# Kernel tuning notes

Hardware: AMD Instinct MI355X
Metric: run time of the kernel (lower is better)

The kernel has to match this reference:

```python
import jax, jax.numpy as jnp
import numpy as np

H = 64; W = 64; P = 16; NPH = 4; NPW = 4; PH = 16; PW = 16; ZD = 32; HD = 1024; UD = 3; B = 256


def affine_grid(theta, Ho, Wo):
    # torch F.affine_grid, align_corners=False. theta [N,2,3] -> grid [N,Ho,Wo,2]
    xs = (2.0 * jnp.arange(Wo, dtype=theta.dtype) + 1.0) / Wo - 1.0
    ys = (2.0 * jnp.arange(Ho, dtype=theta.dtype) + 1.0) / Ho - 1.0
    X, Y = jnp.meshgrid(xs, ys)  # [Ho,Wo] each, x varies along last axis
    base = jnp.stack([X, Y, jnp.ones_like(X)], axis=-1)  # [Ho,Wo,3]
    return jnp.einsum('nij,hwj->nhwi', theta, base)


def grid_sample(img, grid):
    # torch F.grid_sample bilinear, padding_mode='zeros', align_corners=False
    # img [N,H,W], grid [N,Ho,Wo,2] in [-1,1]
    Hi, Wi = img.shape[1], img.shape[2]
    x = (grid[..., 0] + 1.0) * Wi / 2.0 - 0.5
    y = (grid[..., 1] + 1.0) * Hi / 2.0 - 0.5
    x0 = jnp.floor(x); y0 = jnp.floor(y)
    wx = x - x0; wy = y - y0

    def gather(ix, iy):
        valid = (ix >= 0) & (ix < Wi) & (iy >= 0) & (iy < Hi)
        ixc = jnp.clip(ix, 0, Wi - 1).astype(jnp.int32)
        iyc = jnp.clip(iy, 0, Hi - 1).astype(jnp.int32)
        v = jax.vmap(lambda im, yy, xx: im[yy, xx])(img, iyc, ixc)
        return jnp.where(valid, v, 0.0)

    return (gather(x0, y0) * (1 - wx) * (1 - wy)
            + gather(x0 + 1, y0) * wx * (1 - wy)
            + gather(x0, y0 + 1) * (1 - wx) * wy
            + gather(x0 + 1, y0 + 1) * wx * wy)


def rot_tr(u):
    # rotTrMatrix: u [N,3] (angle, tx, ty) -> [N,2,3]
    c = jnp.cos(u[:, 0]); s = jnp.sin(u[:, 0])
    R = jnp.stack([jnp.stack([c, -s], -1), jnp.stack([s, c], -1)], -2)  # [N,2,2]
    return jnp.concatenate([R, u[:, 1:3, None]], axis=2)


def anchor_theta():
    # anchor_move: identity rotation + per-part grid-cell-center translations
    tx = (np.arange(NPW) * (W / NPW) + W / NPW / 2) / W - 0.5
    ty = (np.arange(NPH) * (H / NPH) + H / NPH / 2) / H - 0.5
    th = np.tile(np.concatenate([np.eye(2), np.zeros((2, 1))], axis=1)[None], (P, 1, 1)).astype(np.float32)
    for k in range(P):
        th[k, 0, 2] = tx[k % NPW]
        th[k, 1, 2] = ty[k // NPW]
    return jnp.asarray(th)


def forward(inputs, W1, b1, W2, b2, Wum, bum, Wuv, buv, Wgm, bgm, Wgv, bgv, Wz, M, eps_u, eps_g):
    hid = jax.nn.relu(inputs.reshape(-1, H * W) @ W1 + b1)
    hid = jax.nn.relu(hid @ W2 + b2)
    # global transform distribution (note: F.threshold(x,-6,6) -> 6 where x<=-6)
    gmu = jnp.tanh(hid @ Wgm + bgm)
    gpre = hid @ Wgv + bgv
    gvar = jnp.exp(jnp.where(gpre > -6.0, gpre, 6.0))
    gu = gmu + gvar * eps_g  # sample_u uses mu + var*eps (var, not std) as in source
    # per-part transform distribution (F.threshold(x,-6,-6) -> clamp below at -6)
    umu = jnp.tanh(hid @ Wum + bum)
    upre = hid @ Wuv + buv
    uvar = jnp.exp(jnp.where(upre > -6.0, upre, -6.0))
    u = (umu + uvar * eps_u).reshape(-1, UD)  # [B*P,3]
    # decode parts (input is ones, as in source)
    parts = jax.nn.sigmoid(jnp.ones((B, ZD), inputs.dtype) @ Wz).reshape(B * P, PH, PW)
    padh = (H - PH) // 2; padw = (W - PW) // 2
    parts = jnp.pad(parts, ((0, 0), (padh, H - PH - padh), (padw, W - PW - padw)))
    # anchor placement of parts and kernel masks
    th_a = jnp.tile(anchor_theta(), (B, 1, 1))  # [B*P,2,3], part-minor ordering
    g_a = affine_grid(th_a, H, W)
    parts = grid_sample(parts, g_a)                     # [B*P,H,W]
    KM = grid_sample(M[:B * P].reshape(B * P, H, W), g_a)
    # per-part rotation+translation for parts; translation-only for kernel
    theta = rot_tr(u)                                   # [B*P,2,3]
    g = affine_grid(theta, H, W)
    eye = jnp.broadcast_to(jnp.eye(2, dtype=theta.dtype), (B * P, 2, 2))
    theta_K = jnp.concatenate([eye, theta[:, :, 2:3]], axis=2)
    g_K = affine_grid(theta_K, H, W)
    KM = grid_sample(KM, g_K).reshape(B, P, H, W)
    xp = grid_sample(parts, g).reshape(B, P, H, W)
    # masked weighted compositing
    num = jnp.sum(xp * KM, axis=1)
    den = jnp.sum(KM, axis=1)
    den = jnp.where(den == 0.0, 1.0, den)
    x = num / den
    # global transform
    theta_g = rot_tr(gu)
    g_g = affine_grid(theta_g, H, W)
    return grid_sample(x, g_g)[:, None]  # [B,1,H,W]


def setup_inputs() -> dict:
    key = jax.random.key(0)
    ks = jax.random.split(key, 18)

    def lin(k, fin, fout):
        return jax.random.normal(k, (fin, fout), jnp.float32) / np.sqrt(fin)

    return {
        'inputs': jax.random.uniform(ks[0], (B, H * W), jnp.float32),
        'W1': lin(ks[1], H * W, HD), 'b1': jnp.zeros((HD,), jnp.float32),
        'W2': lin(ks[2], HD, HD), 'b2': jnp.zeros((HD,), jnp.float32),
        'Wum': lin(ks[3], HD, P * UD), 'bum': jnp.zeros((P * UD,), jnp.float32),
        'Wuv': lin(ks[4], HD, P * UD), 'buv': jnp.zeros((P * UD,), jnp.float32),
        'Wgm': lin(ks[5], HD, UD), 'bgm': jnp.zeros((UD,), jnp.float32),
        'Wgv': lin(ks[6], HD, UD), 'bgv': jnp.zeros((UD,), jnp.float32),
        'Wz': lin(ks[7], ZD, P * PH * PW),
        'M': jax.random.uniform(ks[8], (B * P, 1, H, W), jnp.float32),
        'eps_u': jax.random.normal(ks[9], (B, P * UD), jnp.float32),
        'eps_g': jax.random.normal(ks[10], (B, UD), jnp.float32),
    }


def reference(inputs, W1, b1, W2, b2, Wum, bum, Wuv, buv, Wgm, bgm, Wgv, bgv, Wz, M, eps_u, eps_g):
    return forward(inputs, W1, b1, W2, b2, Wum, bum, Wuv, buv, Wgm, bgm, Wgv, bgv, Wz, M, eps_u, eps_g)
```

## Files before the change

kernel.cpp:

```cpp
#include <hip/hip_runtime.h>
#include <math.h>

#define SPLITK 8

typedef __bf16 bf16x8 __attribute__((ext_vector_type(8)));
typedef float  f32x4  __attribute__((ext_vector_type(4)));
typedef float  f32x16 __attribute__((ext_vector_type(16)));

__device__ inline unsigned short bf16rne(float x) {
    unsigned int u = __float_as_uint(x);
    unsigned int r = u + 0x7FFFu + ((u >> 16) & 1u);
    return (unsigned short)(r >> 16);
}
__device__ inline float bf16tof(unsigned short h) {
    return __uint_as_float(((unsigned int)h) << 16);
}

__global__ __launch_bounds__(256) void prep_all(
    const float* __restrict__ inputs,
    const float* __restrict__ W1, const float* __restrict__ W2,
    const float* __restrict__ Wum, const float* __restrict__ Wuv,
    const float* __restrict__ Wgm, const float* __restrict__ Wgv,
    const float* __restrict__ Wz,
    unsigned short* __restrict__ Ahi, unsigned short* __restrict__ Alo,
    unsigned short* __restrict__ W1Thi, unsigned short* __restrict__ W1Tlo,
    unsigned short* __restrict__ W2Thi, unsigned short* __restrict__ W2Tlo,
    float* __restrict__ WT, float* __restrict__ partsb)
{
    __shared__ float t[32][33];
    int bid = blockIdx.x;
    int tid = threadIdx.x;
    if (bid < 4096 || (bid >= 5120 && bid < 6144)) {
        const float* W = (bid < 4096) ? W1 : W2;
        unsigned short* Thi = (bid < 4096) ? W1Thi : W2Thi;
        unsigned short* Tlo = (bid < 4096) ? W1Tlo : W2Tlo;
        int K = (bid < 4096) ? 4096 : 1024;
        int b2 = (bid < 4096) ? bid : (bid - 5120);
        int n0 = (b2 & 31) * 32, k0 = (b2 >> 5) * 32;
        int c = tid & 31, r0 = tid >> 5;
#pragma unroll
        for (int i = 0; i < 4; i++)
            t[r0 + 8 * i][c] = W[(size_t)(k0 + r0 + 8 * i) * 1024 + n0 + c];
        __syncthreads();
        int kk = tid & 31, n1 = tid >> 5;
#pragma unroll
        for (int i = 0; i < 4; i++) {
            float x = t[kk][n1 + 8 * i];
            unsigned short h = bf16rne(x);
            unsigned short l = bf16rne(x - bf16tof(h));
            size_t o = (size_t)(n0 + n1 + 8 * i) * K + k0 + kk;
            Thi[o] = h;
            Tlo[o] = l;
        }
    } else if (bid < 5120) {
        int id = ((bid - 4096) * 256 + tid) * 4;
        float4 x = *(const float4*)(inputs + id);
        ushort4 h, l;
        h.x = bf16rne(x.x); l.x = bf16rne(x.x - bf16tof(h.x));
        h.y = bf16rne(x.y); l.y = bf16rne(x.y - bf16tof(h.y));
        h.z = bf16rne(x.z); l.z = bf16rne(x.z - bf16tof(h.z));
        h.w = bf16rne(x.w); l.w = bf16rne(x.w - bf16tof(h.w));
        *(ushort4*)(Ahi + id) = h;
        *(ushort4*)(Alo + id) = l;
    } else if (bid < 6552) {
        int id = (bid - 6144) * 256 + tid;
        int o = id >> 10;
        int k = id & 1023;
        float v;
        if (o < 48)       v = Wum[k * 48 + o];
        else if (o < 96)  v = Wuv[k * 48 + (o - 48)];
        else if (o < 99)  v = Wgm[k * 3 + (o - 96)];
        else              v = Wgv[k * 3 + (o - 99)];
        WT[id] = v;
    } else {
        int idx = (bid - 6552) * 256 + tid;
        float s = 0.f;
#pragma unroll
        for (int z = 0; z < 32; z++) s += Wz[z * 4096 + idx];
        partsb[idx] = 1.f / (1.f + expf(-s));
    }
}

__global__ __launch_bounds__(256) void gemm_bf16x3(
    const unsigned short* __restrict__ Ahi, const unsigned short* __restrict__ Alo,
    const unsigned short* __restrict__ Bhi, const unsigned short* __restrict__ Blo,
    float* __restrict__ psum, int K, int kchunk)
{
    __shared__ unsigned short Ah[4096], Al[4096], Bh[4096], Bl[4096];
    int tid = threadIdx.x;
    int n0 = blockIdx.x * 64, m0 = blockIdx.y * 64;
    int kb = blockIdx.z * kchunk;
    int wid = tid >> 6, lane = tid & 63;
    int wm = wid & 1, wn = wid >> 1;
    int lr = lane & 31, hi = lane >> 5;

    int r0 = tid >> 3, ch0 = tid & 7;
    int r1 = (tid + 256) >> 3, ch1 = (tid + 256) & 7;
    int l0 = r0 * 64 + 8 * (ch0 ^ (r0 & 7));
    int l1 = r1 * 64 + 8 * (ch1 ^ (r1 & 7));
    size_t ga0 = (size_t)(m0 + r0) * K + kb + ch0 * 8;
    size_t ga1 = (size_t)(m0 + r1) * K + kb + ch1 * 8;
    size_t gb0 = (size_t)(n0 + r0) * K + kb + ch0 * 8;
    size_t gb1 = (size_t)(n0 + r1) * K + kb + ch1 * 8;

    f32x16 acc_hh = {}, acc_hl = {}, acc_lh = {};

    int nkt = kchunk >> 6;
    uint4 vah0, vah1, val0, val1, vbh0, vbh1, vbl0, vbl1;
    vah0 = *(const uint4*)(Ahi + ga0);
    vah1 = *(const uint4*)(Ahi + ga1);
    val0 = *(const uint4*)(Alo + ga0);
    val1 = *(const uint4*)(Alo + ga1);
    vbh0 = *(const uint4*)(Bhi + gb0);
    vbh1 = *(const uint4*)(Bhi + gb1);
    vbl0 = *(const uint4*)(Blo + gb0);
    vbl1 = *(const uint4*)(Blo + gb1);

    int basea = (wm * 32 + lr) * 64;
    int baseb = (wn * 32 + lr) * 64;
    int sw = lr & 7;

    for (int kt = 0; kt < nkt; kt++) {
        __syncthreads();
        *(uint4*)(Ah + l0) = vah0;
        *(uint4*)(Ah + l1) = vah1;
        *(uint4*)(Al + l0) = val0;
        *(uint4*)(Al + l1) = val1;
        *(uint4*)(Bh + l0) = vbh0;
        *(uint4*)(Bh + l1) = vbh1;
        *(uint4*)(Bl + l0) = vbl0;
        *(uint4*)(Bl + l1) = vbl1;
        __syncthreads();
        if (kt + 1 < nkt) {
            size_t o = (size_t)(kt + 1) * 64;
            vah0 = *(const uint4*)(Ahi + ga0 + o);
            vah1 = *(const uint4*)(Ahi + ga1 + o);
            val0 = *(const uint4*)(Alo + ga0 + o);
            val1 = *(const uint4*)(Alo + ga1 + o);
            vbh0 = *(const uint4*)(Bhi + gb0 + o);
            vbh1 = *(const uint4*)(Bhi + gb1 + o);
            vbl0 = *(const uint4*)(Blo + gb0 + o);
            vbl1 = *(const uint4*)(Blo + gb1 + o);
        }
#pragma unroll
        for (int s = 0; s < 4; s++) {
            int cidx = 8 * (((s << 1) + hi) ^ sw);
            bf16x8 afh = *(const bf16x8*)(Ah + basea + cidx);
            bf16x8 afl = *(const bf16x8*)(Al + basea + cidx);
            bf16x8 bfh = *(const bf16x8*)(Bh + baseb + cidx);
            bf16x8 bfl = *(const bf16x8*)(Bl + baseb + cidx);
            acc_hh = __builtin_amdgcn_mfma_f32_32x32x16_bf16(afh, bfh, acc_hh, 0, 0, 0);
            acc_hl = __builtin_amdgcn_mfma_f32_32x32x16_bf16(afh, bfl, acc_hl, 0, 0, 0);
            acc_lh = __builtin_amdgcn_mfma_f32_32x32x16_bf16(afl, bfh, acc_lh, 0, 0, 0);
        }
    }

    float* op = psum + (size_t)blockIdx.z * (256 * 1024);
    int colg = n0 + wn * 32 + lr;
#pragma unroll
    for (int r = 0; r < 16; r++) {
        int rowl = (r & 3) + 8 * (r >> 2) + 4 * hi;
        float v = acc_hh[r] + acc_hl[r] + acc_lh[r];
        op[(size_t)(m0 + wm * 32 + rowl) * 1024 + colg] = v;
    }
}

__global__ __launch_bounds__(256) void reduce_bias_relu_split(
    const float* __restrict__ psum, const float* __restrict__ bias,
    unsigned short* __restrict__ hi, unsigned short* __restrict__ lo)
{
    int i = (blockIdx.x * 256 + threadIdx.x) * 4;
    float4 v = *(const float4*)(psum + i);
#pragma unroll
    for (int s = 1; s < SPLITK; s++) {
        float4 t = *(const float4*)(psum + (size_t)s * 262144 + i);
        v.x += t.x; v.y += t.y; v.z += t.z; v.w += t.w;
    }
    float4 bb = *(const float4*)(bias + (i & 1023));
    v.x = fmaxf(v.x + bb.x, 0.f);
    v.y = fmaxf(v.y + bb.y, 0.f);
    v.z = fmaxf(v.z + bb.z, 0.f);
    v.w = fmaxf(v.w + bb.w, 0.f);
    ushort4 h, l;
    h.x = bf16rne(v.x); l.x = bf16rne(v.x - bf16tof(h.x));
    h.y = bf16rne(v.y); l.y = bf16rne(v.y - bf16tof(h.y));
    h.z = bf16rne(v.z); l.z = bf16rne(v.z - bf16tof(h.z));
    h.w = bf16rne(v.w); l.w = bf16rne(v.w - bf16tof(h.w));
    *(ushort4*)(hi + i) = h;
    *(ushort4*)(lo + i) = l;
}

__global__ __launch_bounds__(512) void heads_v3(
    const float* __restrict__ psum, const float* __restrict__ b2,
    const float* __restrict__ WT,
    const float* __restrict__ bum, const float* __restrict__ buv,
    const float* __restrict__ bgm, const float* __restrict__ bgv,
    const float* __restrict__ eps_u, const float* __restrict__ eps_g,
    float* __restrict__ u_out, float* __restrict__ gu_out)
{
    int b = blockIdx.x;
    int tid = threadIdx.x;
    int w = tid >> 6, l = tid & 63;

    float4 hr[4];
#pragma unroll
    for (int i = 0; i < 4; i++) {
        int k = b * 1024 + i * 256 + l * 4;
        float4 acc = *(const float4*)(psum + k);
#pragma unroll
        for (int s = 1; s < SPLITK; s++) {
            float4 t = *(const float4*)(psum + (size_t)s * 262144 + k);
            acc.x += t.x; acc.y += t.y; acc.z += t.z; acc.w += t.w;
        }
        float4 bb = *(const float4*)(b2 + i * 256 + l * 4);
        acc.x = fmaxf(acc.x + bb.x, 0.f);
        acc.y = fmaxf(acc.y + bb.y, 0.f);
        acc.z = fmaxf(acc.z + bb.z, 0.f);
        acc.w = fmaxf(acc.w + bb.w, 0.f);
        hr[i] = acc;
    }

    int o = w;
    int rm = (o < 48) ? o : (48 + o);
    int rv = (o < 48) ? (o + 48) : (51 + o);
    float4 wm[4], wv[4];
    {
        const float* wp = WT + rm * 1024 + l * 4;
#pragma unroll
        for (int i = 0; i < 4; i++) wm[i] = *(const float4*)(wp + i * 256);
        wp = WT + rv * 1024 + l * 4;
#pragma unroll
        for (int i = 0; i < 4; i++) wv[i] = *(const float4*)(wp + i * 256);
    }

    while (o < 51) {
        int onext = o + 8;
        float4 wmn[4], wvn[4];
        if (onext < 51) {
            int rm2 = (onext < 48) ? onext : (48 + onext);
            int rv2 = (onext < 48) ? (onext + 48) : (51 + onext);
            const float* wp = WT + rm2 * 1024 + l * 4;
#pragma unroll
            for (int i = 0; i < 4; i++) wmn[i] = *(const float4*)(wp + i * 256);
            wp = WT + rv2 * 1024 + l * 4;
#pragma unroll
            for (int i = 0; i < 4; i++) wvn[i] = *(const float4*)(wp + i * 256);
        }
        float am = 0.f, av = 0.f;
#pragma unroll
        for (int i = 0; i < 4; i++) {
            am = fmaf(hr[i].x, wm[i].x, am);
            am = fmaf(hr[i].y, wm[i].y, am);
            am = fmaf(hr[i].z, wm[i].z, am);
            am = fmaf(hr[i].w, wm[i].w, am);
            av = fmaf(hr[i].x, wv[i].x, av);
            av = fmaf(hr[i].y, wv[i].y, av);
            av = fmaf(hr[i].z, wv[i].z, av);
            av = fmaf(hr[i].w, wv[i].w, av);
        }
#pragma unroll
        for (int s = 32; s; s >>= 1) {
            am += __shfl_xor(am, s, 64);
            av += __shfl_xor(av, s, 64);
        }
        if (l == 0) {
            if (o < 48) {
                float umu = tanhf(am + bum[o]);
                float uvar = expf(fmaxf(av + buv[o], -6.f));
                u_out[b * 48 + o] = umu + uvar * eps_u[b * 48 + o];
            } else {
                int n = o - 48;
                float gmu = tanhf(am + bgm[n]);
                float gpre = av + bgv[n];
                float gvar = expf(gpre > -6.f ? gpre : 6.f);
                gu_out[b * 3 + n] = gmu + gvar * eps_g[b * 3 + n];
            }
        }
#pragma unroll
        for (int i = 0; i < 4; i++) { wm[i] = wmn[i]; wv[i] = wvn[i]; }
        o = onext;
    }
}

__global__ __launch_bounds__(1024) void composite_final(
    const float* __restrict__ M, const float* __restrict__ parts,
    const float* __restrict__ u, const float* __restrict__ gu,
    float* __restrict__ out)
{
    __shared__ float patch[4096];
    __shared__ float plane[2][4096];
    __shared__ float pc[16], psn[16], ptx[16], pty[16], pwx[16], pwy[16];
    __shared__ int pix[16], piy[16];
    int b = blockIdx.x;
    int tid = threadIdx.x;

    for (int i = tid; i < 4096; i += 1024) patch[i] = parts[i];
    if (tid < 16) {
        const float* up = u + (b * 16 + tid) * 3;
        float ang = up[0];
        pc[tid] = cosf(ang);
        psn[tid] = sinf(ang);
        float tx = up[1], ty = up[2];
        ptx[tid] = tx;
        pty[tid] = ty;
        float ax = fminf(fmaxf(32.f * tx, -16384.f), 16384.f);
        float fax = floorf(ax);
        pwx[tid] = ax - fax;
        pix[tid] = (int)fax;
        float ay = fminf(fmaxf(32.f * ty, -16384.f), 16384.f);
        float fay = floorf(ay);
        pwy[tid] = ay - fay;
        piy[tid] = (int)fay;
    }

    const float* Mb = M + ((size_t)(b * 16) << 12);
    ((float4*)plane[0])[tid] = ((const float4*)Mb)[tid];
    float4 pfn = ((const float4*)(Mb + 4096))[tid];
    __syncthreads();

    int j = tid & 63;
    int i0 = (tid >> 6) * 4;
    float xnv = (float)(2 * j + 1) * (1.f / 64.f) - 1.f;
    float ynv0 = (float)(2 * i0 + 1) * (1.f / 64.f) - 1.f;

    float num[4] = {}, den[4] = {};

    for (int p = 0; p < 16; p++) {
        int cur = p & 1;
        if (p + 1 < 16) ((float4*)plane[1 - cur])[tid] = pfn;
        if (p + 2 < 16) pfn = ((const float4*)(Mb + ((size_t)(p + 2) << 12)))[tid];

        int dx = 8 * (p & 3) - 12;
        int dy = 8 * (p >> 2) - 12;
        float c = pc[p], s = psn[p], tx = ptx[p], ty = pty[p];
        float wx = pwx[p], wy = pwy[p];
        int ix = pix[p], iy = piy[p];
        int iY = iy + dy;

        int x0 = j + ix;
        int X = x0 + dx;
        bool vc0 = ((unsigned)x0 < 64u) && ((unsigned)X < 64u);
        bool vc1 = ((unsigned)(x0 + 1) < 64u) && ((unsigned)(X + 1) < 64u);
        float w0 = vc0 ? (1.f - wx) : 0.f;
        float w1 = vc1 ? wx : 0.f;
        int Xc0 = min(max(X, 0), 63);
        int Xc1 = min(max(X + 1, 0), 63);

        const float* pl = plane[cur];
        float R[5];
#pragma unroll
        for (int r = 0; r < 5; r++) {
            int i = i0 + r;
            int ri = i + iY;
            bool vr = ((unsigned)(i + iy) < 64u) && ((unsigned)ri < 64u);
            int ric = min(max(ri, 0), 63);
            const float* row = pl + (ric << 6);
            float val = fmaf(w0, row[Xc0], w1 * row[Xc1]);
            R[r] = vr ? val : 0.f;
        }

        float gx0 = fmaf(-s, ynv0, fmaf(c, xnv, tx));
        float gy0 = fmaf(c, ynv0, fmaf(s, xnv, ty));
        float xs = fmaf(gx0, 32.f, 31.5f);
        float ysv = fmaf(gy0, 32.f, 31.5f);
        int ox = 24 - dx, oy = 24 - dy;
        float oxf = (float)ox, oyf = (float)oy;
        const float* pp = patch + (p << 8);
#pragma unroll
        for (int r = 0; r < 4; r++) {
            float km = fmaf(wy, R[r + 1] - R[r], R[r]);
            den[r] += km;

            if (xs >= oxf - 1.f && xs < oxf + 16.f &&
                ysv >= oyf - 1.f && ysv < oyf + 16.f) {
                float xf = floorf(xs), yf = floorf(ysv);
                float wxx = xs - xf, wyy = ysv - yf;
                int a0 = (int)yf - oy;
                int b0c = (int)xf - ox;
                float v00 = 0.f, v10 = 0.f, v01 = 0.f, v11 = 0.f;
                if ((unsigned)a0 < 16u) {
                    const float* pr = pp + a0 * 16;
                    if ((unsigned)b0c < 16u) v00 = pr[b0c];
                    if ((unsigned)(b0c + 1) < 16u) v10 = pr[b0c + 1];
                }
                if ((unsigned)(a0 + 1) < 16u) {
                    const float* pr = pp + (a0 + 1) * 16;
                    if ((unsigned)b0c < 16u) v01 = pr[b0c];
                    if ((unsigned)(b0c + 1) < 16u) v11 = pr[b0c + 1];
                }
                float top = fmaf(wxx, v10 - v00, v00);
                float bot = fmaf(wxx, v11 - v01, v01);
                float xp = fmaf(wyy, bot - top, top);
                num[r] = fmaf(xp, km, num[r]);
            }
            xs -= s;
            ysv += c;
        }
        __syncthreads();
    }

    float* xl = plane[0];
#pragma unroll
    for (int r = 0; r < 4; r++) {
        float d = (den[r] == 0.f) ? 1.f : den[r];
        xl[(i0 + r) * 64 + j] = num[r] / d;
    }
    __syncthreads();

    float ang = gu[b * 3 + 0], gtx = gu[b * 3 + 1], gty = gu[b * 3 + 2];
    float cg = cosf(ang), sg = sinf(ang);
    float* ob = out + ((size_t)b << 12);
#pragma unroll
    for (int r = 0; r < 4; r++) {
        int i = i0 + r;
        float ynv = (float)(2 * i + 1) * (1.f / 64.f) - 1.f;
        float gx = cg * xnv - sg * ynv + gtx;
        float gy = sg * xnv + cg * ynv + gty;
        gx = fminf(fmaxf(gx, -8.f), 8.f);
        gy = fminf(fmaxf(gy, -8.f), 8.f);
        float xs = fmaf(gx, 32.f, 31.5f);
        float ysv = fmaf(gy, 32.f, 31.5f);
        float xf = floorf(xs), yf = floorf(ysv);
        float wx = xs - xf, wy = ysv - yf;
        int x0 = (int)xf, y0 = (int)yf;
        float v00 = 0.f, v10 = 0.f, v01 = 0.f, v11 = 0.f;
        bool vx0 = (unsigned)x0 < 64u, vx1 = (unsigned)(x0 + 1) < 64u;
        if ((unsigned)y0 < 64u) {
            const float* row = xl + y0 * 64;
            if (vx0) v00 = row[x0];
            if (vx1) v10 = row[x0 + 1];
        }
        if ((unsigned)(y0 + 1) < 64u) {
            const float* row = xl + (y0 + 1) * 64;
            if (vx0) v01 = row[x0];
            if (vx1) v11 = row[x0 + 1];
        }
        float top = fmaf(wx, v10 - v00, v00);
        float bot = fmaf(wx, v11 - v01, v01);
        ob[i * 64 + j] = fmaf(wy, bot - top, top);
    }
}

extern "C" void kernel_launch(void* const* d_in, const int* in_sizes, int n_in,
                              void* d_out, int out_size, void* d_ws, size_t ws_size,
                              hipStream_t stream)
{
    (void)in_sizes; (void)n_in; (void)out_size; (void)ws_size;
    const float* inputs = (const float*)d_in[0];
    const float* W1  = (const float*)d_in[1];
    const float* b1  = (const float*)d_in[2];
    const float* W2  = (const float*)d_in[3];
    const float* b2  = (const float*)d_in[4];
    const float* Wum = (const float*)d_in[5];
    const float* bum = (const float*)d_in[6];
    const float* Wuv = (const float*)d_in[7];
    const float* buv = (const float*)d_in[8];
    const float* Wgm = (const float*)d_in[9];
    const float* bgm = (const float*)d_in[10];
    const float* Wgv = (const float*)d_in[11];
    const float* bgv = (const float*)d_in[12];
    const float* Wz  = (const float*)d_in[13];
    const float* Mm  = (const float*)d_in[14];
    const float* eps_u = (const float*)d_in[15];
    const float* eps_g = (const float*)d_in[16];

    float* ws = (float*)d_ws;
    float* psum      = ws;
    float* u_buf     = ws + 2097152;
    float* gu_buf    = u_buf + 12288;
    float* parts_buf = gu_buf + 768;
    float* WTh_buf   = parts_buf + 4096;
    unsigned short* us = (unsigned short*)(WTh_buf + 104448);
    unsigned short* Ahi   = us;
    unsigned short* Alo   = Ahi + 1048576;
    unsigned short* W1Thi = Alo + 1048576;
    unsigned short* W1Tlo = W1Thi + 4194304;
    unsigned short* W2Thi = W1Tlo + 4194304;
    unsigned short* W2Tlo = W2Thi + 1048576;
    unsigned short* H1hi  = W2Tlo + 1048576;
    unsigned short* H1lo  = H1hi + 262144;

    prep_all<<<6568, 256, 0, stream>>>(inputs, W1, W2, Wum, Wuv, Wgm, Wgv, Wz,
                                       Ahi, Alo, W1Thi, W1Tlo, W2Thi, W2Tlo,
                                       WTh_buf, parts_buf);

    gemm_bf16x3<<<dim3(16, 4, SPLITK), 256, 0, stream>>>(Ahi, Alo, W1Thi, W1Tlo,
                                                         psum, 4096, 4096 / SPLITK);
    reduce_bias_relu_split<<<256, 256, 0, stream>>>(psum, b1, H1hi, H1lo);
    gemm_bf16x3<<<dim3(16, 4, SPLITK), 256, 0, stream>>>(H1hi, H1lo, W2Thi, W2Tlo,
                                                         psum, 1024, 1024 / SPLITK);
    heads_v3<<<256, 512, 0, stream>>>(psum, b2, WTh_buf, bum, buv, bgm, bgv,
                                      eps_u, eps_g, u_buf, gu_buf);
    composite_final<<<256, 1024, 0, stream>>>(Mm, parts_buf, u_buf, gu_buf,
                                              (float*)d_out);
}
```

Before: 198.0 us.

## Fuse heads projection into composite kernel via shared-memory handoff

Merges the heads kernel (split-K reduction of the second GEMM, bias+ReLU, and the 51 head dot products) into the compositing kernel. The per-batch latent values are passed through shared memory instead of global u/gu buffers. This removes one kernel launch and a global round trip. In exchange, each 1024-thread block runs the head dot products and extra syncs before starting compositing, which adds to that block's critical path.

```diff
diff --git a/kernel.cpp b/kernel.cpp
--- a/kernel.cpp
+++ b/kernel.cpp
@@ -2,17 +2,17 @@
 #include <math.h>
 
 #define SPLITK 8
+#define PSUM_STRIDE 262144
 
 typedef __bf16 bf16x8 __attribute__((ext_vector_type(8)));
-typedef float  f32x4  __attribute__((ext_vector_type(4)));
 typedef float  f32x16 __attribute__((ext_vector_type(16)));
 
-__device__ inline unsigned short bf16rne(float x) {
+__device__ __forceinline__ unsigned short bf16rne(float x) {
     unsigned int u = __float_as_uint(x);
     unsigned int r = u + 0x7FFFu + ((u >> 16) & 1u);
     return (unsigned short)(r >> 16);
 }
-__device__ inline float bf16tof(unsigned short h) {
+__device__ __forceinline__ float bf16tof(unsigned short h) {
     return __uint_as_float(((unsigned int)h) << 16);
 }
 
@@ -155,13 +155,12 @@
         }
     }
 
-    float* op = psum + (size_t)blockIdx.z * (256 * 1024);
+    float* op = psum + (size_t)blockIdx.z * PSUM_STRIDE;
     int colg = n0 + wn * 32 + lr;
 #pragma unroll
     for (int r = 0; r < 16; r++) {
         int rowl = (r & 3) + 8 * (r >> 2) + 4 * hi;
-        float v = acc_hh[r] + acc_hl[r] + acc_lh[r];
-        op[(size_t)(m0 + wm * 32 + rowl) * 1024 + colg] = v;
+        op[(size_t)(m0 + wm * 32 + rowl) * 1024 + colg] = acc_hh[r] + acc_hl[r] + acc_lh[r];
     }
 }
 
@@ -173,7 +172,7 @@
     float4 v = *(const float4*)(psum + i);
 #pragma unroll
     for (int s = 1; s < SPLITK; s++) {
-        float4 t = *(const float4*)(psum + (size_t)s * 262144 + i);
+        float4 t = *(const float4*)(psum + (size_t)s * PSUM_STRIDE + i);
         v.x += t.x; v.y += t.y; v.z += t.z; v.w += t.w;
     }
     float4 bb = *(const float4*)(bias + (i & 1023));
@@ -190,117 +189,95 @@
     *(ushort4*)(lo + i) = l;
 }
 
-__global__ __launch_bounds__(512) void heads_v3(
+__global__ __launch_bounds__(1024) void composite_heads(
     const float* __restrict__ psum, const float* __restrict__ b2,
     const float* __restrict__ WT,
     const float* __restrict__ bum, const float* __restrict__ buv,
     const float* __restrict__ bgm, const float* __restrict__ bgv,
     const float* __restrict__ eps_u, const float* __restrict__ eps_g,
-    float* __restrict__ u_out, float* __restrict__ gu_out)
-{
-    int b = blockIdx.x;
-    int tid = threadIdx.x;
-    int w = tid >> 6, l = tid & 63;
-
-    float4 hr[4];
-#pragma unroll
-    for (int i = 0; i < 4; i++) {
-        int k = b * 1024 + i * 256 + l * 4;
-        float4 acc = *(const float4*)(psum + k);
-#pragma unroll
-        for (int s = 1; s < SPLITK; s++) {
-            float4 t = *(const float4*)(psum + (size_t)s * 262144 + k);
-            acc.x += t.x; acc.y += t.y; acc.z += t.z; acc.w += t.w;
-        }
-        float4 bb = *(const float4*)(b2 + i * 256 + l * 4);
-        acc.x = fmaxf(acc.x + bb.x, 0.f);
-        acc.y = fmaxf(acc.y + bb.y, 0.f);
-        acc.z = fmaxf(acc.z + bb.z, 0.f);
-        acc.w = fmaxf(acc.w + bb.w, 0.f);
-        hr[i] = acc;
-    }
-
-    int o = w;
-    int rm = (o < 48) ? o : (48 + o);
-    int rv = (o < 48) ? (o + 48) : (51 + o);
-    float4 wm[4], wv[4];
-    {
-        const float* wp = WT + rm * 1024 + l * 4;
-#pragma unroll
-        for (int i = 0; i < 4; i++) wm[i] = *(const float4*)(wp + i * 256);
-        wp = WT + rv * 1024 + l * 4;
-#pragma unroll
-        for (int i = 0; i < 4; i++) wv[i] = *(const float4*)(wp + i * 256);
-    }
-
-    while (o < 51) {
-        int onext = o + 8;
-        float4 wmn[4], wvn[4];
-        if (onext < 51) {
-            int rm2 = (onext < 48) ? onext : (48 + onext);
-            int rv2 = (onext < 48) ? (onext + 48) : (51 + onext);
-            const float* wp = WT + rm2 * 1024 + l * 4;
-#pragma unroll
-            for (int i = 0; i < 4; i++) wmn[i] = *(const float4*)(wp + i * 256);
-            wp = WT + rv2 * 1024 + l * 4;
-#pragma unroll
-            for (int i = 0; i < 4; i++) wvn[i] = *(const float4*)(wp + i * 256);
-        }
-        float am = 0.f, av = 0.f;
-#pragma unroll
-        for (int i = 0; i < 4; i++) {
-            am = fmaf(hr[i].x, wm[i].x, am);
-            am = fmaf(hr[i].y, wm[i].y, am);
-            am = fmaf(hr[i].z, wm[i].z, am);
-            am = fmaf(hr[i].w, wm[i].w, am);
-            av = fmaf(hr[i].x, wv[i].x, av);
-            av = fmaf(hr[i].y, wv[i].y, av);
-            av = fmaf(hr[i].z, wv[i].z, av);
-            av = fmaf(hr[i].w, wv[i].w, av);
-        }
-#pragma unroll
-        for (int s = 32; s; s >>= 1) {
-            am += __shfl_xor(am, s, 64);
-            av += __shfl_xor(av, s, 64);
-        }
-        if (l == 0) {
-            if (o < 48) {
-                float umu = tanhf(am + bum[o]);
-                float uvar = expf(fmaxf(av + buv[o], -6.f));
-                u_out[b * 48 + o] = umu + uvar * eps_u[b * 48 + o];
-            } else {
-                int n = o - 48;
-                float gmu = tanhf(am + bgm[n]);
-                float gpre = av + bgv[n];
-                float gvar = expf(gpre > -6.f ? gpre : 6.f);
-                gu_out[b * 3 + n] = gmu + gvar * eps_g[b * 3 + n];
-            }
-        }
-#pragma unroll
-        for (int i = 0; i < 4; i++) { wm[i] = wmn[i]; wv[i] = wvn[i]; }
-        o = onext;
-    }
-}
-
-__global__ __launch_bounds__(1024) void composite_final(
     const float* __restrict__ M, const float* __restrict__ parts,
-    const float* __restrict__ u, const float* __restrict__ gu,
     float* __restrict__ out)
 {
     __shared__ float patch[4096];
     __shared__ float plane[2][4096];
+    __shared__ float h2[1024];
+    __shared__ float u_raw[51];
     __shared__ float pc[16], psn[16], ptx[16], pty[16], pwx[16], pwy[16];
     __shared__ int pix[16], piy[16];
     int b = blockIdx.x;
     int tid = threadIdx.x;
 
+    {
+        float v = psum[(size_t)b * 1024 + tid];
+#pragma unroll
+        for (int s = 1; s < SPLITK; s++)
+            v += psum[(size_t)s * PSUM_STRIDE + (size_t)b * 1024 + tid];
+        h2[tid] = fmaxf(v + b2[tid], 0.f);
+    }
     for (int i = tid; i < 4096; i += 1024) patch[i] = parts[i];
+    __syncthreads();
+
+    {
+        int w = tid >> 6, l = tid & 63;
+        const float4* h4 = (const float4*)h2;
+        float4 hr0 = h4[l], hr1 = h4[64 + l], hr2 = h4[128 + l], hr3 = h4[192 + l];
+        for (int o = w; o < 51; o += 16) {
+            int rm = (o < 48) ? o : (48 + o);
+            int rv = (o < 48) ? (o + 48) : (51 + o);
+            const float* wpm = WT + rm * 1024 + l * 4;
+            const float* wpv = WT + rv * 1024 + l * 4;
+            float4 wm0 = *(const float4*)(wpm);
+            float4 wm1 = *(const float4*)(wpm + 256);
+            float4 wm2 = *(const float4*)(wpm + 512);
+            float4 wm3 = *(const float4*)(wpm + 768);
+            float4 wv0 = *(const float4*)(wpv);
+            float4 wv1 = *(const float4*)(wpv + 256);
+            float4 wv2 = *(const float4*)(wpv + 512);
+            float4 wv3 = *(const float4*)(wpv + 768);
+            float am = 0.f, av = 0.f;
+            am = fmaf(hr0.x, wm0.x, am); am = fmaf(hr0.y, wm0.y, am);
+            am = fmaf(hr0.z, wm0.z, am); am = fmaf(hr0.w, wm0.w, am);
+            av = fmaf(hr0.x, wv0.x, av); av = fmaf(hr0.y, wv0.y, av);
+            av = fmaf(hr0.z, wv0.z, av); av = fmaf(hr0.w, wv0.w, av);
+            am = fmaf(hr1.x, wm1.x, am); am = fmaf(hr1.y, wm1.y, am);
+            am = fmaf(hr1.z, wm1.z, am); am = fmaf(hr1.w, wm1.w, am);
+            av = fmaf(hr1.x, wv1.x, av); av = fmaf(hr1.y, wv1.y, av);
+            av = fmaf(hr1.z, wv1.z, av); av = fmaf(hr1.w, wv1.w, av);
+            am = fmaf(hr2.x, wm2.x, am); am = fmaf(hr2.y, wm2.y, am);
+            am = fmaf(hr2.z, wm2.z, am); am = fmaf(hr2.w, wm2.w, am);
+            av = fmaf(hr2.x, wv2.x, av); av = fmaf(hr2.y, wv2.y, av);
+            av = fmaf(hr2.z, wv2.z, av); av = fmaf(hr2.w, wv2.w, av);
+            am = fmaf(hr3.x, wm3.x, am); am = fmaf(hr3.y, wm3.y, am);
+            am = fmaf(hr3.z, wm3.z, am); am = fmaf(hr3.w, wm3.w, am);
+            av = fmaf(hr3.x, wv3.x, av); av = fmaf(hr3.y, wv3.y, av);
+            av = fmaf(hr3.w, wv3.w, av); av = fmaf(hr3.z, wv3.z, av);
+#pragma unroll
+            for (int s = 32; s; s >>= 1) {
+                am += __shfl_xor(am, s, 64);
+                av += __shfl_xor(av, s, 64);
+            }
+            if (l == 0) {
+                if (o < 48) {
+                    float umu = tanhf(am + bum[o]);
+                    float uvar = expf(fmaxf(av + buv[o], -6.f));
+                    u_raw[o] = umu + uvar * eps_u[b * 48 + o];
+                } else {
+                    int n = o - 48;
+                    float gmu = tanhf(am + bgm[n]);
+                    float gpre = av + bgv[n];
+                    float gvar = expf(gpre > -6.f ? gpre : 6.f);
+                    u_raw[o] = gmu + gvar * eps_g[b * 3 + n];
+                }
+            }
+        }
+    }
+    __syncthreads();
+
     if (tid < 16) {
-        const float* up = u + (b * 16 + tid) * 3;
-        float ang = up[0];
+        float ang = u_raw[tid * 3 + 0];
+        float tx = u_raw[tid * 3 + 1], ty = u_raw[tid * 3 + 2];
         pc[tid] = cosf(ang);
         psn[tid] = sinf(ang);
-        float tx = up[1], ty = up[2];
         ptx[tid] = tx;
         pty[tid] = ty;
         float ax = fminf(fmaxf(32.f * tx, -16384.f), 16384.f);
@@ -312,7 +289,6 @@
         pwy[tid] = ay - fay;
         piy[tid] = (int)fay;
     }
-
     const float* Mb = M + ((size_t)(b * 16) << 12);
     ((float4*)plane[0])[tid] = ((const float4*)Mb)[tid];
     float4 pfn = ((const float4*)(Mb + 4096))[tid];
@@ -324,10 +300,11 @@
     float ynv0 = (float)(2 * i0 + 1) * (1.f / 64.f) - 1.f;
 
     float num[4] = {}, den[4] = {};
+    float* pl_cur = plane[0];
+    float* pl_nxt = plane[1];
 
     for (int p = 0; p < 16; p++) {
-        int cur = p & 1;
-        if (p + 1 < 16) ((float4*)plane[1 - cur])[tid] = pfn;
+        if (p + 1 < 16) ((float4*)pl_nxt)[tid] = pfn;
         if (p + 2 < 16) pfn = ((const float4*)(Mb + ((size_t)(p + 2) << 12)))[tid];
 
         int dx = 8 * (p & 3) - 12;
@@ -346,7 +323,7 @@
         int Xc0 = min(max(X, 0), 63);
         int Xc1 = min(max(X + 1, 0), 63);
 
-        const float* pl = plane[cur];
+        const float* pl = pl_cur;
         float R[5];
 #pragma unroll
         for (int r = 0; r < 5; r++) {
@@ -397,6 +374,7 @@
             ysv += c;
         }
         __syncthreads();
+        float* tmp = pl_cur; pl_cur = pl_nxt; pl_nxt = tmp;
     }
 
     float* xl = plane[0];
@@ -407,7 +385,7 @@
     }
     __syncthreads();
 
-    float ang = gu[b * 3 + 0], gtx = gu[b * 3 + 1], gty = gu[b * 3 + 2];
+    float ang = u_raw[48], gtx = u_raw[49], gty = u_raw[50];
     float cg = cosf(ang), sg = sinf(ang);
     float* ob = out + ((size_t)b << 12);
 #pragma unroll
@@ -466,9 +444,7 @@
 
     float* ws = (float*)d_ws;
     float* psum      = ws;
-    float* u_buf     = ws + 2097152;
-    float* gu_buf    = u_buf + 12288;
-    float* parts_buf = gu_buf + 768;
+    float* parts_buf = psum + 8 * PSUM_STRIDE;
     float* WTh_buf   = parts_buf + 4096;
     unsigned short* us = (unsigned short*)(WTh_buf + 104448);
     unsigned short* Ahi   = us;
@@ -489,8 +465,7 @@
     reduce_bias_relu_split<<<256, 256, 0, stream>>>(psum, b1, H1hi, H1lo);
     gemm_bf16x3<<<dim3(16, 4, SPLITK), 256, 0, stream>>>(H1hi, H1lo, W2Thi, W2Tlo,
                                                          psum, 1024, 1024 / SPLITK);
-    heads_v3<<<256, 512, 0, stream>>>(psum, b2, WTh_buf, bum, buv, bgm, bgv,
-                                      eps_u, eps_g, u_buf, gu_buf);
-    composite_final<<<256, 1024, 0, stream>>>(Mm, parts_buf, u_buf, gu_buf,
-                                              (float*)d_out);
-}
+    composite_heads<<<256, 1024, 0, stream>>>(psum, b2, WTh_buf, bum, buv,
+                                              bgm, bgv, eps_u, eps_g,
+                                              Mm, parts_buf, (float*)d_out);
+}
```

Result: faster. 193.8 us (-2.1%).
